# Performance work log

Hardware: AMD Instinct MI355X
Metric: run time of the kernel (lower is better)

The kernel has to match this reference:

```python
import jax, jax.numpy as jnp
import numpy as np

N = 4096      # nodes
D = 256       # input_dim
OUT = 256     # output_dim
K = 4         # num_kernels
TOPK = 16
CHEB_T = 2
ROW_TEMP = 1.0
EPS = 1e-9


def setup_inputs() -> dict:
    key = jax.random.key(0)
    ks = jax.random.split(key, 6)
    X = jax.random.normal(ks[0], (N, D), dtype=jnp.float32)
    L_k = jax.random.normal(ks[1], (K, D, D), dtype=jnp.float32) * 0.02
    alpha = jnp.ones((K,), dtype=jnp.float32)
    theta = jax.random.normal(ks[2], (CHEB_T + 1, D), dtype=jnp.float32) * 0.02
    rho_raw = jnp.zeros((), dtype=jnp.float32)
    proj_w = jax.random.normal(ks[3], (OUT, D), dtype=jnp.float32) / np.float32(np.sqrt(D))
    proj_b = jnp.zeros((OUT,), dtype=jnp.float32)
    v0 = jax.random.normal(ks[4], (N, 1), dtype=jnp.float32)  # power-iteration init
    return dict(X=X, L_k=L_k, alpha=alpha, theta=theta, rho_raw=rho_raw,
                proj_w=proj_w, proj_b=proj_b, v0=v0)


def reference(X, L_k, alpha, theta, rho_raw, proj_w, proj_b, v0):
    n, d = X.shape
    k = L_k.shape[0]
    # 1) kernel stack: A_k = X L_k X^T / sqrt(D), row softmax  -> (K,N,N)
    A = jnp.einsum('nd,kde,me->knm', X, L_k, X) / jnp.sqrt(jnp.float32(d))
    H_stack = jax.nn.softmax(A / max(ROW_TEMP, 1e-6), axis=-1)
    w = jax.nn.softmax(alpha)[:, None, None]
    H_fused = (H_stack * w).sum(0)                               # (N,N)
    # 2) soft incidence via per-row top-k + renormalize, scattered into B (N, K*N)
    vals, idx = jax.lax.top_k(H_stack, TOPK)                     # (K,N,TOPK)
    vals = vals / (vals.sum(-1, keepdims=True) + EPS)
    E = k * n
    cols = jnp.arange(k)[:, None, None] * n + jnp.arange(n)[None, :, None]
    cols = jnp.broadcast_to(cols, idx.shape)
    B = jnp.zeros((n, E), X.dtype).at[idx.reshape(-1), cols.reshape(-1)].set(vals.reshape(-1))
    W = jnp.ones((E,), X.dtype)
    # 3) hypergraph Laplacian L = I - Dv^{-1/2} B W De^{-1} B^T Dv^{-1/2}
    De = B.sum(0) + EPS
    Dv = (B * W[None, :]).sum(1) + EPS
    Dv_is = 1.0 / jnp.sqrt(Dv)
    S = (B * (W / De)[None, :]) @ B.T                            # (N,N)
    S_norm = Dv_is[:, None] * S * Dv_is[None, :]
    L = jnp.eye(n, dtype=X.dtype) - S_norm
    # 4) lambda_max via power iteration on detached L (constant, as in torch)
    Ld = jax.lax.stop_gradient(L)
    v = v0 / (jnp.linalg.norm(v0) + EPS)
    for _ in range(5):
        v = Ld @ v
        v = v / (jnp.linalg.norm(v) + EPS)
    lam = jnp.maximum((v.T @ (Ld @ v)).squeeze(), jnp.float32(1e-3))
    lam = jax.lax.stop_gradient(lam)
    # Chebyshev filter
    L_tilde = (2.0 / lam) * L - jnp.eye(n, dtype=X.dtype)
    out = X * theta[0][None, :]
    T0 = X
    T1 = L_tilde @ X
    out = out + T1 * theta[1][None, :]
    for t in range(2, CHEB_T + 1):
        T2 = 2.0 * (L_tilde @ T1) - T0
        out = out + T2 * theta[t][None, :]
        T0, T1 = T1, T2
    Z_spec = jax.nn.elu(out)
    # 5) residual blend with kernel diffusion
    Z_kern = H_fused @ X
    rho = jax.nn.sigmoid(rho_raw)
    Z_mix = rho * Z_spec + (1.0 - rho) * Z_kern
    # 6) final projection
    return Z_mix @ proj_w.T + proj_b[None, :]
```

## Files before the change

### kernel.cpp

```cpp
#include <hip/hip_runtime.h>
#include <math.h>

#define N_ 4096
#define D_ 256
#define K_ 4
#define TK_ 16
#define E_ (K_ * N_)
#define NENT_ (E_ * TK_)

typedef unsigned short u16;
typedef unsigned int u32;
typedef __attribute__((ext_vector_type(8))) short bf16x8;
typedef __attribute__((ext_vector_type(4))) float f32x4;

__device__ __forceinline__ u16 bf16_rne(float x) {
  u32 u = __float_as_uint(x);
  u32 r = u + 0x7FFFu + ((u >> 16) & 1u);
  return (u16)(r >> 16);
}


__global__ void scalars_kernel(const float* __restrict__ alpha,
                               const float* __restrict__ rho_raw,
                               float* __restrict__ scal) {
  if (threadIdx.x == 0) {
    float m = alpha[0];
    for (int k = 1; k < K_; ++k) m = fmaxf(m, alpha[k]);
    float e[K_]; float s = 0.f;
    for (int k = 0; k < K_; ++k) { e[k] = expf(alpha[k] - m); s += e[k]; }
    for (int k = 0; k < K_; ++k) scal[k] = e[k] / s;
    scal[4] = 1.0f / (1.0f + expf(-rho_raw[0]));
  }
}

__global__ void dvis_kernel(const float* __restrict__ DvAcc, float* __restrict__ Dvis) {
  int i = blockIdx.x * 256 + threadIdx.x;
  Dvis[i] = 1.0f / sqrtf(DvAcc[i] + 1e-9f);
}

__global__ void ew_scale(const float* __restrict__ M, const float* __restrict__ Dvis,
                         float* __restrict__ U) {
  int i = blockIdx.x * 256 + threadIdx.x;
  U[i] = Dvis[i >> 8] * M[i];
}

__global__ void cvt_split4(const float* __restrict__ in, u16* __restrict__ hi,
                           u16* __restrict__ lo) {
  int i = (blockIdx.x * 256 + threadIdx.x) * 4;
  float4 v = *(const float4*)(in + i);
  u16 h0 = bf16_rne(v.x), h1 = bf16_rne(v.y), h2 = bf16_rne(v.z), h3 = bf16_rne(v.w);
  float f0 = __uint_as_float((u32)h0 << 16), f1 = __uint_as_float((u32)h1 << 16);
  float f2 = __uint_as_float((u32)h2 << 16), f3 = __uint_as_float((u32)h3 << 16);
  u16 l0 = bf16_rne(v.x - f0), l1 = bf16_rne(v.y - f1);
  u16 l2 = bf16_rne(v.z - f2), l3 = bf16_rne(v.w - f3);
  *(uint2*)(hi + i) = make_uint2((u32)h0 | ((u32)h1 << 16), (u32)h2 | ((u32)h3 << 16));
  *(uint2*)(lo + i) = make_uint2((u32)l0 | ((u32)l1 << 16), (u32)l2 | ((u32)l3 << 16));
}

__global__ __launch_bounds__(256) void transpose_split(const float* __restrict__ X,
                                                       u16* __restrict__ ht,
                                                       u16* __restrict__ lt) {
  __shared__ float tile[32][33];
  const int tx = threadIdx.x & 31, ty = threadIdx.x >> 5;
  const int d0 = blockIdx.x * 32, n0 = blockIdx.y * 32;
#pragma unroll
  for (int q = 0; q < 4; ++q)
    tile[ty + q * 8][tx] = X[(size_t)(n0 + ty + q * 8) * D_ + d0 + tx];
  __syncthreads();
#pragma unroll
  for (int q = 0; q < 4; ++q) {
    int dd = ty + q * 8;
    float v = tile[tx][dd];
    u16 h = bf16_rne(v);
    float hf = __uint_as_float((u32)h << 16);
    u16 l = bf16_rne(v - hf);
    ht[(size_t)(d0 + dd) * N_ + n0 + tx] = h;
    lt[(size_t)(d0 + dd) * N_ + n0 + tx] = l;
  }
}

__global__ __launch_bounds__(256) void gemm_nn64_split(const float* __restrict__ A,
                                                       const float* __restrict__ B,
                                                       u16* __restrict__ Ch,
                                                       u16* __restrict__ Cl,
                                                       int Kdim, int lda, int ldb, int ldc) {
  __shared__ float As[16][68];
  __shared__ float Bs[16][68];
  const int tid = threadIdx.x;
  const int bm = blockIdx.x * 64, bn = blockIdx.y * 64;
  const int lrA = tid >> 2, lcA = (tid & 3) * 4;
  const int rrB = tid >> 4, ccB = (tid & 15) * 4;
  const int tx = tid & 15, ty = tid >> 4;
  const float* Ap = A + (size_t)(bm + lrA) * lda + lcA;
  const float* Bp = B + (size_t)rrB * ldb + bn + ccB;
  float acc[4][4] = {};
  for (int k0 = 0; k0 < Kdim; k0 += 16) {
    float4 av = *(const float4*)(Ap + k0);
    float4 bv = *(const float4*)(Bp + (size_t)k0 * ldb);
    __syncthreads();
    As[lcA + 0][lrA] = av.x; As[lcA + 1][lrA] = av.y;
    As[lcA + 2][lrA] = av.z; As[lcA + 3][lrA] = av.w;
    *(float4*)&Bs[rrB][ccB] = bv;
    __syncthreads();
#pragma unroll
    for (int kk = 0; kk < 16; ++kk) {
      float a[4], b[4];
      *(float4*)a = *(const float4*)&As[kk][ty * 4];
      *(float4*)b = *(const float4*)&Bs[kk][tx * 4];
#pragma unroll
      for (int i = 0; i < 4; ++i)
#pragma unroll
        for (int j = 0; j < 4; ++j) acc[i][j] += a[i] * b[j];
    }
  }
#pragma unroll
  for (int i = 0; i < 4; ++i) {
    int row = bm + ty * 4 + i;
    u16 h[4], lo[4];
#pragma unroll
    for (int j = 0; j < 4; ++j) {
      h[j] = bf16_rne(acc[i][j]);
      lo[j] = bf16_rne(acc[i][j] - __uint_as_float((u32)h[j] << 16));
    }
    size_t base = (size_t)row * ldc + bn + tx * 4;
    *(uint2*)(Ch + base) = make_uint2((u32)h[0] | ((u32)h[1] << 16), (u32)h[2] | ((u32)h[3] << 16));
    *(uint2*)(Cl + base) = make_uint2((u32)lo[0] | ((u32)lo[1] << 16), (u32)lo[2] | ((u32)lo[3] << 16));
  }
}

__global__ __launch_bounds__(256) void gemm_nt64_bias(const float* __restrict__ A,
                                                      const float* __restrict__ B,
                                                      const float* __restrict__ bias,
                                                      float* __restrict__ C,
                                                      int Kdim, int lda, int ldb, int ldc) {
  __shared__ float As[16][68];
  __shared__ float Bs[16][68];
  const int tid = threadIdx.x;
  const int bm = blockIdx.x * 64, bn = blockIdx.y * 64;
  const int lr = tid >> 2, lc = (tid & 3) * 4;
  const int tx = tid & 15, ty = tid >> 4;
  const float* Ap = A + (size_t)(bm + lr) * lda + lc;
  const float* Bp = B + (size_t)(bn + lr) * ldb + lc;
  float acc[4][4] = {};
  for (int k0 = 0; k0 < Kdim; k0 += 16) {
    float4 av = *(const float4*)(Ap + k0);
    float4 bv = *(const float4*)(Bp + k0);
    __syncthreads();
    As[lc + 0][lr] = av.x; As[lc + 1][lr] = av.y; As[lc + 2][lr] = av.z; As[lc + 3][lr] = av.w;
    Bs[lc + 0][lr] = bv.x; Bs[lc + 1][lr] = bv.y; Bs[lc + 2][lr] = bv.z; Bs[lc + 3][lr] = bv.w;
    __syncthreads();
#pragma unroll
    for (int kk = 0; kk < 16; ++kk) {
      float a[4], b[4];
      *(float4*)a = *(const float4*)&As[kk][ty * 4];
      *(float4*)b = *(const float4*)&Bs[kk][tx * 4];
#pragma unroll
      for (int i = 0; i < 4; ++i)
#pragma unroll
        for (int j = 0; j < 4; ++j) acc[i][j] += a[i] * b[j];
    }
  }
#pragma unroll
  for (int i = 0; i < 4; ++i) {
    int row = bm + ty * 4 + i;
    float4 o;
    o.x = acc[i][0] + bias[bn + tx * 4 + 0];
    o.y = acc[i][1] + bias[bn + tx * 4 + 1];
    o.z = acc[i][2] + bias[bn + tx * 4 + 2];
    o.w = acc[i][3] + bias[bn + tx * 4 + 3];
    *(float4*)(C + (size_t)row * ldc + bn + tx * 4) = o;
  }
}


__global__ __launch_bounds__(256) void scores_mfma(const u16* __restrict__ Ahg,
                                                   const u16* __restrict__ Alg,
                                                   const u16* __restrict__ Bhg,
                                                   const u16* __restrict__ Blg,
                                                   float* __restrict__ C, float scale) {
  __shared__ char smem[32768];
  char* pAh = smem;
  char* pAl = smem + 16384;
  const int tid = threadIdx.x;
  const int bm = blockIdx.x * 128, bn = blockIdx.y * 128;
  const int w = tid >> 6, l = tid & 63;
  const int wr = (w >> 1) * 64, wc = (w & 1) * 64;
  const int srow = tid >> 3, scol = (tid & 7) * 8;
  const int lb = l & 15, lke = (l >> 4) * 8;
  const u16* bh0 = Bhg + (size_t)(bn + wc + 0  + lb) * D_ + lke;
  const u16* bh1 = Bhg + (size_t)(bn + wc + 16 + lb) * D_ + lke;
  const u16* bh2 = Bhg + (size_t)(bn + wc + 32 + lb) * D_ + lke;
  const u16* bh3 = Bhg + (size_t)(bn + wc + 48 + lb) * D_ + lke;
  const size_t dlo = (size_t)(Blg - Bhg);
  f32x4 acc[4][4];
#pragma unroll
  for (int i = 0; i < 4; ++i)
#pragma unroll
    for (int j = 0; j < 4; ++j) { acc[i][j][0] = 0.f; acc[i][j][1] = 0.f; acc[i][j][2] = 0.f; acc[i][j][3] = 0.f; }

  for (int c = 0; c < 4; ++c) {
    const int k0 = c * 64;
    uint4 ah[4], al[4];
#pragma unroll
    for (int ii = 0; ii < 4; ++ii) {
      int r = srow + ii * 32;
      ah[ii] = *(const uint4*)(Ahg + (size_t)(bm + r) * D_ + k0 + scol);
      al[ii] = *(const uint4*)(Alg + (size_t)(bm + r) * D_ + k0 + scol);
    }
    __syncthreads();
#pragma unroll
    for (int ii = 0; ii < 4; ++ii) {
      int r = srow + ii * 32;
      int off = r * 128 + ((scol * 2) ^ ((r & 7) << 4));
      *(uint4*)(pAh + off) = ah[ii];
      *(uint4*)(pAl + off) = al[ii];
    }
    __syncthreads();
#pragma unroll
    for (int kk = 0; kk < 2; ++kk) {
      const int kb = kk * 64 + ((l >> 4) << 4);
      const int ge = k0 + kk * 32;
      bf16x8 fbh[4], fbl[4];
      fbh[0] = *(const bf16x8*)(bh0 + ge); fbl[0] = *(const bf16x8*)(bh0 + dlo + ge);
      fbh[1] = *(const bf16x8*)(bh1 + ge); fbl[1] = *(const bf16x8*)(bh1 + dlo + ge);
      fbh[2] = *(const bf16x8*)(bh2 + ge); fbl[2] = *(const bf16x8*)(bh2 + dlo + ge);
      fbh[3] = *(const bf16x8*)(bh3 + ge); fbl[3] = *(const bf16x8*)(bh3 + dlo + ge);
#pragma unroll
      for (int i = 0; i < 4; ++i) {
        int ra = wr + i * 16 + lb;
        int oa = ra * 128 + (kb ^ ((ra & 7) << 4));
        bf16x8 fah = *(const bf16x8*)(pAh + oa);
        bf16x8 fal = *(const bf16x8*)(pAl + oa);
#pragma unroll
        for (int j = 0; j < 4; ++j) {
          acc[i][j] = __builtin_amdgcn_mfma_f32_16x16x32_bf16(fah, fbh[j], acc[i][j], 0, 0, 0);
          acc[i][j] = __builtin_amdgcn_mfma_f32_16x16x32_bf16(fah, fbl[j], acc[i][j], 0, 0, 0);
          acc[i][j] = __builtin_amdgcn_mfma_f32_16x16x32_bf16(fal, fbh[j], acc[i][j], 0, 0, 0);
        }
      }
    }
  }
  float* Cs = (float*)smem;
  const int cr = (l >> 4) * 4, cc = l & 15;
#pragma unroll
  for (int p = 0; p < 2; ++p) {
    __syncthreads();
    if ((w >> 1) == p) {
#pragma unroll
      for (int i = 0; i < 4; ++i)
#pragma unroll
        for (int r = 0; r < 4; ++r) {
          int rl = i * 16 + cr + r;
          int sw = ((rl >> 2) & 3) << 4;
#pragma unroll
          for (int j = 0; j < 4; ++j) {
            int cl = wc + j * 16 + cc;
            Cs[rl * 128 + (cl ^ sw)] = acc[i][j][r] * scale;
          }
        }
    }
    __syncthreads();
#pragma unroll
    for (int ii = 0; ii < 8; ++ii) {
      int rl = ii * 8 + (tid >> 5);
      int c4 = (tid & 31) * 4;
      float4 v = *(float4*)&Cs[rl * 128 + (c4 ^ (((rl >> 2) & 3) << 4))];
      *(float4*)(C + (size_t)(bm + p * 64 + rl) * N_ + bn + c4) = v;
    }
  }
}

__global__ __launch_bounds__(256) void zkern_mfma(const float* __restrict__ S,
                                                  const float* __restrict__ rowmax,
                                                  const float* __restrict__ rowZ,
                                                  const u16* __restrict__ BhT,
                                                  const u16* __restrict__ BlT,
                                                  float* __restrict__ Zpart,
                                                  const float* __restrict__ scal,
                                                  int kidx, int kchunk) {
  __shared__ char smem[32768];
  char* pAh = smem;
  char* pAl = smem + 16384;
  const int tid = threadIdx.x;
  const int bm = blockIdx.x * 128, bn = blockIdx.y * 128;
  const int kz = blockIdx.z;
  const int w = tid >> 6, l = tid & 63;
  const int wr = (w >> 1) * 64, wc = (w & 1) * 64;
  const int arow = tid >> 4, acol = (tid & 15) * 4;
  const int lb = l & 15, lke = (l >> 4) * 8;
  const u16* bh0 = BhT + (size_t)(bn + wc + 0  + lb) * N_ + lke;
  const u16* bh1 = BhT + (size_t)(bn + wc + 16 + lb) * N_ + lke;
  const u16* bh2 = BhT + (size_t)(bn + wc + 32 + lb) * N_ + lke;
  const u16* bh3 = BhT + (size_t)(bn + wc + 48 + lb) * N_ + lke;
  const size_t dlo = (size_t)(BlT - BhT);
  float rm[8];
#pragma unroll
  for (int ii = 0; ii < 8; ++ii) rm[ii] = rowmax[bm + arow + ii * 16];
  f32x4 acc[4][4];
#pragma unroll
  for (int i = 0; i < 4; ++i)
#pragma unroll
    for (int j = 0; j < 4; ++j) { acc[i][j][0] = 0.f; acc[i][j][1] = 0.f; acc[i][j][2] = 0.f; acc[i][j][3] = 0.f; }

  const int nchunk = kchunk >> 6;
  for (int c = 0; c < nchunk; ++c) {
    const int k0 = kz * kchunk + c * 64;
    uint2 eh[8], el[8];
#pragma unroll
    for (int ii = 0; ii < 8; ++ii) {
      int r = arow + ii * 16;
      float4 s = *(const float4*)(S + (size_t)(bm + r) * N_ + k0 + acol);
      float e0 = expf(s.x - rm[ii]), e1 = expf(s.y - rm[ii]);
      float e2 = expf(s.z - rm[ii]), e3 = expf(s.w - rm[ii]);
      u16 h0 = bf16_rne(e0), h1 = bf16_rne(e1), h2 = bf16_rne(e2), h3 = bf16_rne(e3);
      u16 l0 = bf16_rne(e0 - __uint_as_float((u32)h0 << 16));
      u16 l1 = bf16_rne(e1 - __uint_as_float((u32)h1 << 16));
      u16 l2 = bf16_rne(e2 - __uint_as_float((u32)h2 << 16));
      u16 l3 = bf16_rne(e3 - __uint_as_float((u32)h3 << 16));
      eh[ii] = make_uint2((u32)h0 | ((u32)h1 << 16), (u32)h2 | ((u32)h3 << 16));
      el[ii] = make_uint2((u32)l0 | ((u32)l1 << 16), (u32)l2 | ((u32)l3 << 16));
    }
    __syncthreads();
#pragma unroll
    for (int ii = 0; ii < 8; ++ii) {
      int r = arow + ii * 16;
      int off = r * 128 + ((acol * 2) ^ ((r & 7) << 4));
      *(uint2*)(pAh + off) = eh[ii];
      *(uint2*)(pAl + off) = el[ii];
    }
    __syncthreads();
#pragma unroll
    for (int kk = 0; kk < 2; ++kk) {
      const int kb = kk * 64 + ((l >> 4) << 4);
      const int ge = k0 + kk * 32;
      bf16x8 fbh[4], fbl[4];
      fbh[0] = *(const bf16x8*)(bh0 + ge); fbl[0] = *(const bf16x8*)(bh0 + dlo + ge);
      fbh[1] = *(const bf16x8*)(bh1 + ge); fbl[1] = *(const bf16x8*)(bh1 + dlo + ge);
      fbh[2] = *(const bf16x8*)(bh2 + ge); fbl[2] = *(const bf16x8*)(bh2 + dlo + ge);
      fbh[3] = *(const bf16x8*)(bh3 + ge); fbl[3] = *(const bf16x8*)(bh3 + dlo + ge);
#pragma unroll
      for (int i = 0; i < 4; ++i) {
        int ra = wr + i * 16 + lb;
        int oa = ra * 128 + (kb ^ ((ra & 7) << 4));
        bf16x8 fah = *(const bf16x8*)(pAh + oa);
        bf16x8 fal = *(const bf16x8*)(pAl + oa);
#pragma unroll
        for (int j = 0; j < 4; ++j) {
          acc[i][j] = __builtin_amdgcn_mfma_f32_16x16x32_bf16(fah, fbh[j], acc[i][j], 0, 0, 0);
          acc[i][j] = __builtin_amdgcn_mfma_f32_16x16x32_bf16(fah, fbl[j], acc[i][j], 0, 0, 0);
          acc[i][j] = __builtin_amdgcn_mfma_f32_16x16x32_bf16(fal, fbh[j], acc[i][j], 0, 0, 0);
        }
      }
    }
  }
  const float wk = scal[kidx];
  float* Zp = Zpart + (size_t)kz * N_ * D_;
  float* Cs = (float*)smem;
  const int cr = (l >> 4) * 4, cc = l & 15;
#pragma unroll
  for (int p = 0; p < 2; ++p) {
    __syncthreads();
    if ((w >> 1) == p) {
#pragma unroll
      for (int i = 0; i < 4; ++i)
#pragma unroll
        for (int r = 0; r < 4; ++r) {
          int rl = i * 16 + cr + r;
          int sw = ((rl >> 2) & 3) << 4;
#pragma unroll
          for (int j = 0; j < 4; ++j) {
            int cl = wc + j * 16 + cc;
            Cs[rl * 128 + (cl ^ sw)] = acc[i][j][r];
          }
        }
    }
    __syncthreads();
#pragma unroll
    for (int ii = 0; ii < 8; ++ii) {
      int rl = ii * 8 + (tid >> 5);
      int c4 = (tid & 31) * 4;
      int row = bm + p * 64 + rl;
      float sc = wk / rowZ[row];
      float4 v = *(float4*)&Cs[rl * 128 + (c4 ^ (((rl >> 2) & 3) << 4))];
      float* zb = Zp + (size_t)row * D_ + bn + c4;
      float4 z = *(float4*)zb;
      z.x += sc * v.x; z.y += sc * v.y; z.z += sc * v.z; z.w += sc * v.w;
      *(float4*)zb = z;
    }
  }
}

__global__ __launch_bounds__(256) void rowstats_topk(const float* __restrict__ S,
                                                     float* __restrict__ rowmax,
                                                     float* __restrict__ rowZ,
                                                     float* __restrict__ tkv,
                                                     int* __restrict__ tki) {
  const int row = blockIdx.x, tid = threadIdx.x;
  const int wid = tid >> 6, lane = tid & 63;
  __shared__ int hist[1024];
  __shared__ int P[256];
  __shared__ float cval[256];
  __shared__ int cgi[256];
  __shared__ int ccnt;
  __shared__ int binlo_s;
  __shared__ float rv[4];
  __shared__ float stk[TK_];
  __shared__ int itk[TK_];
  __shared__ float tv16[TK_];
  __shared__ float mzs[3];

  hist[tid] = 0; hist[tid + 256] = 0; hist[tid + 512] = 0; hist[tid + 768] = 0;
  if (tid == 0) ccnt = 0;

  const float4* Sp = (const float4*)(S + (size_t)row * N_);
  float r[16];
  float lmax = -3.4e38f;
#pragma unroll
  for (int it = 0; it < 4; ++it) {
    float4 v = Sp[tid + it * 256];
    r[it * 4 + 0] = v.x; r[it * 4 + 1] = v.y; r[it * 4 + 2] = v.z; r[it * 4 + 3] = v.w;
    lmax = fmaxf(lmax, fmaxf(fmaxf(v.x, v.y), fmaxf(v.z, v.w)));
  }
#pragma unroll
  for (int off = 32; off; off >>= 1) lmax = fmaxf(lmax, __shfl_xor(lmax, off));
  if (lane == 0) rv[wid] = lmax;
  __syncthreads();
  if (tid == 0) mzs[0] = fmaxf(fmaxf(rv[0], rv[1]), fmaxf(rv[2], rv[3]));
  __syncthreads();
  const float M = mzs[0];
  float ls = 0.f;
#pragma unroll
  for (int j = 0; j < 16; ++j) ls += expf(r[j] - M);
#pragma unroll
  for (int off = 32; off; off >>= 1) ls += __shfl_xor(ls, off);
  if (lane == 0) rv[wid] = ls;
  __syncthreads();
  if (tid == 0) {
    float z = rv[0] + rv[1] + rv[2] + rv[3];
    mzs[1] = z; rowmax[row] = M; rowZ[row] = z;
  }
  __syncthreads();
  const float Z = mzs[1];

#pragma unroll
  for (int j = 0; j < 16; ++j) {
    u32 u = __float_as_uint(r[j]);
    u32 key = (u >> 31) ? ~u : (u | 0x80000000u);
    atomicAdd(&hist[key >> 22], 1);
  }
  __syncthreads();
  const int b0 = tid * 4;
  const int h0 = hist[b0], h1 = hist[b0 + 1], h2 = hist[b0 + 2], h3 = hist[b0 + 3];
  P[tid] = h0 + h1 + h2 + h3;
  __syncthreads();
  for (int o = 1; o < 256; o <<= 1) {
    int v = P[tid] + ((tid + o < 256) ? P[tid + o] : 0);
    __syncthreads();
    P[tid] = v;
    __syncthreads();
  }
  {
    int above = (tid < 255) ? P[tid + 1] : 0;
    int s3 = above + h3, s2 = s3 + h2, s1 = s2 + h1, s0 = s1 + h0;
    if (s3 >= TK_ && above < TK_) binlo_s = b0 + 3;
    else if (s2 >= TK_ && s3 < TK_) binlo_s = b0 + 2;
    else if (s1 >= TK_ && s2 < TK_) binlo_s = b0 + 1;
    else if (s0 >= TK_ && s1 < TK_) binlo_s = b0;
  }
  __syncthreads();
  const u32 kmin = (u32)binlo_s << 22;
#pragma unroll
  for (int j = 0; j < 16; ++j) {
    u32 u = __float_as_uint(r[j]);
    u32 key = (u >> 31) ? ~u : (u | 0x80000000u);
    if (key >= kmin) {
      int p = atomicAdd(&ccnt, 1);
      if (p < 256) {
        cval[p] = r[j];
        cgi[p] = 4 * tid + ((j >> 2) << 10) + (j & 3);
      }
    }
  }
  __syncthreads();
  const int nc = min(ccnt, 256);
  for (int t = 0; t < TK_; ++t) {
    if (tid < 64) {
      float bv = -3.4e38f; int bg = 0x7fffffff, bp = -1;
      for (int p = tid; p < nc; p += 64) {
        float v = cval[p]; int g = cgi[p];
        if (v > bv || (v == bv && g < bg)) { bv = v; bg = g; bp = p; }
      }
#pragma unroll
      for (int off = 32; off; off >>= 1) {
        float ov = __shfl_xor(bv, off);
        int og = __shfl_xor(bg, off);
        int op = __shfl_xor(bp, off);
        if (ov > bv || (ov == bv && og < bg)) { bv = ov; bg = og; bp = op; }
      }
      if (tid == 0) { stk[t] = bv; itk[t] = bg; cval[bp] = -3.4e38f; }
    }
    __syncthreads();
  }
  if (tid < TK_) tv16[tid] = expf(stk[tid] - M) / Z;
  __syncthreads();
  if (tid == 0) { float s = 0.f; for (int q = 0; q < TK_; ++q) s += tv16[q]; mzs[2] = s + 1e-9f; }
  __syncthreads();
  if (tid < TK_) {
    tkv[(size_t)row * TK_ + tid] = tv16[tid] / mzs[2];
    tki[(size_t)row * TK_ + tid] = itk[tid];
  }
}

__global__ void edge_scan(const float* __restrict__ tkv, const int* __restrict__ tki,
                          float* __restrict__ DvAcc, int* __restrict__ cnt,
                          float* __restrict__ invDe) {
  int e = blockIdx.x * 256 + threadIdx.x;
  float s = 0.f;
#pragma unroll
  for (int q = 0; q < TK_; ++q) s += tkv[(size_t)e * TK_ + q];
  invDe[e] = 1.0f / (s + 1e-9f);
#pragma unroll
  for (int q = 0; q < TK_; ++q) {
    int m = tki[(size_t)e * TK_ + q];
    atomicAdd(&DvAcc[m], tkv[(size_t)e * TK_ + q]);
    atomicAdd(&cnt[m], 1);
  }
}

__global__ __launch_bounds__(1024) void scan_offsets(const int* __restrict__ cnt,
                                                     int* __restrict__ off,
                                                     int* __restrict__ cur) {
  __shared__ int part[1024];
  const int t = threadIdx.x;
  const int b = t * 4;
  int c0 = cnt[b], c1 = cnt[b + 1], c2 = cnt[b + 2], c3 = cnt[b + 3];
  part[t] = c0 + c1 + c2 + c3;
  __syncthreads();
  for (int o = 1; o < 1024; o <<= 1) {
    int v = part[t] + ((t >= o) ? part[t - o] : 0);
    __syncthreads();
    part[t] = v;
    __syncthreads();
  }
  int ex = (t == 0) ? 0 : part[t - 1];
  off[b] = ex; off[b + 1] = ex + c0; off[b + 2] = ex + c0 + c1; off[b + 3] = ex + c0 + c1 + c2;
  cur[b] = off[b]; cur[b + 1] = off[b + 1]; cur[b + 2] = off[b + 2]; cur[b + 3] = off[b + 3];
  if (t == 1023) off[N_] = part[1023];
}

__global__ void edge_fill(const float* __restrict__ tkv, const int* __restrict__ tki,
                          int* __restrict__ cur, int* __restrict__ ince,
                          float* __restrict__ incv) {
  int e = blockIdx.x * 256 + threadIdx.x;
#pragma unroll
  for (int q = 0; q < TK_; ++q) {
    int m = tki[(size_t)e * TK_ + q];
    int pos = atomicAdd(&cur[m], 1);
    ince[pos] = e;
    incv[pos] = tkv[(size_t)e * TK_ + q];
  }
}

__global__ void pi_init(const float* __restrict__ v0, const float* __restrict__ Dvis,
                        float* __restrict__ v, float* __restrict__ u) {
  int i = blockIdx.x * 256 + threadIdx.x;
  float x = v0[i];
  v[i] = x; u[i] = Dvis[i] * x;
}

__global__ void pi_ye(const float* __restrict__ u, const float* __restrict__ tkv,
                      const int* __restrict__ tki, const float* __restrict__ invDe,
                      float* __restrict__ ye) {
  int e = blockIdx.x * 256 + threadIdx.x;
  const float* tv = tkv + (size_t)e * TK_;
  const int* ti = tki + (size_t)e * TK_;
  float a = 0.f;
#pragma unroll
  for (int q = 0; q < TK_; ++q) a += tv[q] * u[ti[q]];
  ye[e] = a * invDe[e];
}

__global__ void pi_step(const float* __restrict__ v, const float* __restrict__ ye,
                        const int* __restrict__ off, const int* __restrict__ ince,
                        const float* __restrict__ incv, const float* __restrict__ Dvis,
                        float* __restrict__ vn, float* __restrict__ un) {
  int m = blockIdx.x * 256 + threadIdx.x;
  float z = 0.f;
  int j0 = off[m], j1 = off[m + 1];
  for (int j = j0; j < j1; ++j) z += incv[j] * ye[ince[j]];
  float wv = v[m] - Dvis[m] * z;
  vn[m] = wv; un[m] = Dvis[m] * wv;
}

__global__ __launch_bounds__(256) void pi_final(const float* __restrict__ v,
                                                const float* __restrict__ ye,
                                                const int* __restrict__ off,
                                                const int* __restrict__ ince,
                                                const float* __restrict__ incv,
                                                const float* __restrict__ Dvis,
                                                float* __restrict__ partial) {
  __shared__ float r1[256], r2[256];
  int m = blockIdx.x * 256 + threadIdx.x;
  float z = 0.f;
  int j0 = off[m], j1 = off[m + 1];
  for (int j = j0; j < j1; ++j) z += incv[j] * ye[ince[j]];
  float wv = v[m] - Dvis[m] * z;
  r1[threadIdx.x] = v[m] * wv;
  r2[threadIdx.x] = v[m] * v[m];
  __syncthreads();
  for (int s = 128; s; s >>= 1) {
    if (threadIdx.x < s) { r1[threadIdx.x] += r1[threadIdx.x + s]; r2[threadIdx.x] += r2[threadIdx.x + s]; }
    __syncthreads();
  }
  if (threadIdx.x == 0) { partial[blockIdx.x * 2] = r1[0]; partial[blockIdx.x * 2 + 1] = r2[0]; }
}

__global__ void pi_lam(const float* __restrict__ partial, float* __restrict__ scal) {
  if (threadIdx.x == 0) {
    float s1 = 0.f, s2 = 0.f;
    for (int b = 0; b < N_ / 256; ++b) { s1 += partial[2 * b]; s2 += partial[2 * b + 1]; }
    scal[5] = fmaxf(s1 / s2, 1e-3f);
  }
}

__global__ __launch_bounds__(256) void ye_mat(const float* __restrict__ U,
                                              const float* __restrict__ tkv,
                                              const int* __restrict__ tki,
                                              const float* __restrict__ invDe,
                                              float* __restrict__ Ye) {
  const int e = blockIdx.x, d = threadIdx.x;
  __shared__ float sv[TK_];
  __shared__ int si[TK_];
  if (d < TK_) { sv[d] = tkv[(size_t)e * TK_ + d]; si[d] = tki[(size_t)e * TK_ + d]; }
  __syncthreads();
  float a = 0.f;
#pragma unroll
  for (int q = 0; q < TK_; ++q) a += sv[q] * U[(size_t)si[q] * D_ + d];
  Ye[(size_t)e * D_ + d] = a * invDe[e];
}

__global__ __launch_bounds__(256) void bgather_combine(const float* __restrict__ Ye,
                                                       const int* __restrict__ off,
                                                       const int* __restrict__ ince,
                                                       const float* __restrict__ incv,
                                                       const float* __restrict__ Dvis,
                                                       const float* __restrict__ Mx,
                                                       const float* __restrict__ G,
                                                       const float* __restrict__ scal,
                                                       float* __restrict__ out, int mode) {
  const int m = blockIdx.x, d = threadIdx.x;
  const int j0 = off[m], j1 = off[m + 1];
  float z = 0.f;
  for (int j = j0; j < j1; ++j) z += incv[j] * Ye[(size_t)ince[j] * D_ + d];
  const float lam = scal[5];
  const float c = 2.0f / lam;
  const size_t idx = (size_t)m * D_ + d;
  const float zz = Dvis[m] * z;
  float r;
  if (mode == 1) r = (c - 1.0f) * Mx[idx] - c * zz;
  else           r = (2.0f * c - 2.0f) * Mx[idx] - 2.0f * c * zz - G[idx];
  out[idx] = r;
}

__global__ void mix_kernel(const float* __restrict__ X, const float* __restrict__ T1,
                           const float* __restrict__ T2, const float* __restrict__ theta,
                           const float* __restrict__ Zpart, int splitk,
                           const float* __restrict__ scal, float* __restrict__ Zmix) {
  const int i = blockIdx.x * 256 + threadIdx.x;
  const int d = i & (D_ - 1);
  float cheb = X[i] * theta[d] + T1[i] * theta[D_ + d] + T2[i] * theta[2 * D_ + d];
  float zs = cheb > 0.f ? cheb : expm1f(cheb);
  float zk = 0.f;
  for (int s = 0; s < splitk; ++s) zk += Zpart[(size_t)s * N_ * D_ + i];
  const float rho = scal[4];
  Zmix[i] = rho * zs + (1.0f - rho) * zk;
}


extern "C" void kernel_launch(void* const* d_in, const int* in_sizes, int n_in,
                              void* d_out, int out_size, void* d_ws, size_t ws_size,
                              hipStream_t stream) {
  const float* X       = (const float*)d_in[0];
  const float* L_k     = (const float*)d_in[1];
  const float* alpha   = (const float*)d_in[2];
  const float* theta   = (const float*)d_in[3];
  const float* rho_raw = (const float*)d_in[4];
  const float* proj_w  = (const float*)d_in[5];
  const float* proj_b  = (const float*)d_in[6];
  const float* v0      = (const float*)d_in[7];
  float* out = (float*)d_out;

  char* w = (char*)d_ws;
  size_t o = 0;
  auto alloc = [&](size_t bytes) -> char* {
    char* p = w + o; o += (bytes + 255) & ~(size_t)255; return p;
  };
  float* S     = (float*)alloc((size_t)N_ * N_ * 4);
  u16*   Xh    = (u16*)  alloc((size_t)N_ * D_ * 2);
  u16*   Xl    = (u16*)  alloc((size_t)N_ * D_ * 2);
  u16*   XhT   = (u16*)  alloc((size_t)D_ * N_ * 2);
  u16*   XlT   = (u16*)  alloc((size_t)D_ * N_ * 2);
  u16*   XLh   = (u16*)  alloc((size_t)N_ * D_ * 2);
  u16*   XLl   = (u16*)  alloc((size_t)N_ * D_ * 2);
  float* rowmax= (float*)alloc(N_ * 4);
  float* rowZ  = (float*)alloc(N_ * 4);
  float* tkv   = (float*)alloc((size_t)NENT_ * 4);
  int*   tki   = (int*)  alloc((size_t)NENT_ * 4);
  float* invDe = (float*)alloc(E_ * 4);
  float* DvAcc = (float*)alloc(N_ * 4);
  float* Dvis  = (float*)alloc(N_ * 4);
  int*   cnt   = (int*)  alloc(N_ * 4);
  int*   off   = (int*)  alloc((N_ + 1) * 4);
  int*   cur   = (int*)  alloc(N_ * 4);
  int*   ince  = (int*)  alloc((size_t)NENT_ * 4);
  float* incv  = (float*)alloc((size_t)NENT_ * 4);
  float* va    = (float*)alloc(N_ * 4);
  float* ua    = (float*)alloc(N_ * 4);
  float* vbuf  = (float*)alloc(N_ * 4);
  float* ubuf  = (float*)alloc(N_ * 4);
  float* yev   = (float*)alloc(E_ * 4);
  float* part  = (float*)alloc((N_ / 256) * 2 * 4);
  float* scal  = (float*)alloc(256);
  int SPLITK = 8;
  while (SPLITK > 1 && o + (size_t)SPLITK * N_ * D_ * 4 > ws_size) SPLITK >>= 1;
  float* Zpart = (float*)alloc((size_t)SPLITK * N_ * D_ * 4);
  const int kchunk = N_ / SPLITK;
  float* U    = S;
  float* Ye   = S + (size_t)N_ * D_;
  float* T1   = Ye + (size_t)E_ * D_;
  float* T2   = T1 + (size_t)N_ * D_;
  float* Zmix = T2 + (size_t)N_ * D_;

  scalars_kernel<<<1, 64, 0, stream>>>(alpha, rho_raw, scal);
  hipMemsetAsync(Zpart, 0, (size_t)SPLITK * N_ * D_ * 4, stream);
  hipMemsetAsync(DvAcc, 0, N_ * 4, stream);
  hipMemsetAsync(cnt, 0, N_ * 4, stream);

  cvt_split4<<<(N_ * D_ / 4) / 256, 256, 0, stream>>>(X, Xh, Xl);
  transpose_split<<<dim3(D_ / 32, N_ / 32), 256, 0, stream>>>(X, XhT, XlT);

  for (int k = 0; k < K_; ++k) {
    gemm_nn64_split<<<dim3(N_ / 64, D_ / 64), 256, 0, stream>>>(
        X, L_k + (size_t)k * D_ * D_, XLh, XLl, D_, D_, D_, D_);
    scores_mfma<<<dim3(N_ / 128, N_ / 128), 256, 0, stream>>>(
        XLh, XLl, Xh, Xl, S, 1.0f / 16.0f);
    rowstats_topk<<<N_, 256, 0, stream>>>(
        S, rowmax, rowZ, tkv + (size_t)k * N_ * TK_, tki + (size_t)k * N_ * TK_);
    zkern_mfma<<<dim3(N_ / 128, D_ / 128, SPLITK), 256, 0, stream>>>(
        S, rowmax, rowZ, XhT, XlT, Zpart, scal, k, kchunk);
  }

  edge_scan<<<E_ / 256, 256, 0, stream>>>(tkv, tki, DvAcc, cnt, invDe);
  dvis_kernel<<<N_ / 256, 256, 0, stream>>>(DvAcc, Dvis);
  scan_offsets<<<1, 1024, 0, stream>>>(cnt, off, cur);
  edge_fill<<<E_ / 256, 256, 0, stream>>>(tkv, tki, cur, ince, incv);

  pi_init<<<N_ / 256, 256, 0, stream>>>(v0, Dvis, va, ua);
  float* vc = va; float* uc = ua; float* vn = vbuf; float* un = ubuf;
  for (int it = 0; it < 5; ++it) {
    pi_ye<<<E_ / 256, 256, 0, stream>>>(uc, tkv, tki, invDe, yev);
    pi_step<<<N_ / 256, 256, 0, stream>>>(vc, yev, off, ince, incv, Dvis, vn, un);
    float* tv = vc; vc = vn; vn = tv;
    float* tu = uc; uc = un; un = tu;
  }
  pi_ye<<<E_ / 256, 256, 0, stream>>>(uc, tkv, tki, invDe, yev);
  pi_final<<<N_ / 256, 256, 0, stream>>>(vc, yev, off, ince, incv, Dvis, part);
  pi_lam<<<1, 64, 0, stream>>>(part, scal);

  ew_scale<<<N_ * D_ / 256, 256, 0, stream>>>(X, Dvis, U);
  ye_mat<<<E_, 256, 0, stream>>>(U, tkv, tki, invDe, Ye);
  bgather_combine<<<N_, 256, 0, stream>>>(Ye, off, ince, incv, Dvis, X, X, scal, T1, 1);
  ew_scale<<<N_ * D_ / 256, 256, 0, stream>>>(T1, Dvis, U);
  ye_mat<<<E_, 256, 0, stream>>>(U, tkv, tki, invDe, Ye);
  bgather_combine<<<N_, 256, 0, stream>>>(Ye, off, ince, incv, Dvis, T1, X, scal, T2, 2);

  mix_kernel<<<N_ * D_ / 256, 256, 0, stream>>>(X, T1, T2, theta, Zpart, SPLITK, scal, Zmix);

  gemm_nt64_bias<<<dim3(N_ / 64, D_ / 64), 256, 0, stream>>>(
      Zmix, proj_w, proj_b, out, D_, D_, D_, D_);
}
```

Before: 1.449 ms.

## Double-buffer LDS A-tiles in scores and zkern MFMA kernels

Both MFMA GEMM kernels now keep two LDS buffers for the A operand. The next chunk's global loads (and, in zkern, its exp/bf16 split) are issued before the current chunk's MFMAs and stored into the alternate buffer afterwards. This cuts one barrier per iteration and is meant to hide global-load latency behind matrix math. In exchange, LDS per block doubles to 64KB and register pressure rises, which may lower occupancy.

Result: faster. 1.276 ms (-11.9%).

```diff
diff --git a/kernel.cpp b/kernel.cpp
--- a/kernel.cpp
+++ b/kernel.cpp
@@ -178,9 +178,7 @@
                                                    const u16* __restrict__ Bhg,
                                                    const u16* __restrict__ Blg,
                                                    float* __restrict__ C, float scale) {
-  __shared__ char smem[32768];
-  char* pAh = smem;
-  char* pAl = smem + 16384;
+  __shared__ char smem[65536];
   const int tid = threadIdx.x;
   const int bm = blockIdx.x * 128, bn = blockIdx.y * 128;
   const int w = tid >> 6, l = tid & 63;
@@ -192,34 +190,51 @@
   const u16* bh2 = Bhg + (size_t)(bn + wc + 32 + lb) * D_ + lke;
   const u16* bh3 = Bhg + (size_t)(bn + wc + 48 + lb) * D_ + lke;
   const size_t dlo = (size_t)(Blg - Bhg);
+  const int aoff[4] = {
+    (srow + 0)  * 128 + ((scol * 2) ^ (((srow + 0)  & 7) << 4)),
+    (srow + 32) * 128 + ((scol * 2) ^ (((srow + 32) & 7) << 4)),
+    (srow + 64) * 128 + ((scol * 2) ^ (((srow + 64) & 7) << 4)),
+    (srow + 96) * 128 + ((scol * 2) ^ (((srow + 96) & 7) << 4)) };
   f32x4 acc[4][4];
 #pragma unroll
   for (int i = 0; i < 4; ++i)
 #pragma unroll
     for (int j = 0; j < 4; ++j) { acc[i][j][0] = 0.f; acc[i][j][1] = 0.f; acc[i][j][2] = 0.f; acc[i][j][3] = 0.f; }
 
+  uint4 ah[4], al[4];
+#pragma unroll
+  for (int ii = 0; ii < 4; ++ii) {
+    int r = srow + ii * 32;
+    ah[ii] = *(const uint4*)(Ahg + (size_t)(bm + r) * D_ + scol);
+    al[ii] = *(const uint4*)(Alg + (size_t)(bm + r) * D_ + scol);
+  }
+  {
+    char* bAh = smem; char* bAl = smem + 16384;
+#pragma unroll
+    for (int ii = 0; ii < 4; ++ii) {
+      *(uint4*)(bAh + aoff[ii]) = ah[ii];
+      *(uint4*)(bAl + aoff[ii]) = al[ii];
+    }
+  }
+  __syncthreads();
+
   for (int c = 0; c < 4; ++c) {
-    const int k0 = c * 64;
-    uint4 ah[4], al[4];
-#pragma unroll
-    for (int ii = 0; ii < 4; ++ii) {
-      int r = srow + ii * 32;
-      ah[ii] = *(const uint4*)(Ahg + (size_t)(bm + r) * D_ + k0 + scol);
-      al[ii] = *(const uint4*)(Alg + (size_t)(bm + r) * D_ + k0 + scol);
-    }
-    __syncthreads();
-#pragma unroll
-    for (int ii = 0; ii < 4; ++ii) {
-      int r = srow + ii * 32;
-      int off = r * 128 + ((scol * 2) ^ ((r & 7) << 4));
-      *(uint4*)(pAh + off) = ah[ii];
-      *(uint4*)(pAl + off) = al[ii];
-    }
-    __syncthreads();
+    char* bAh = smem + ((c & 1) << 15);
+    char* bAl = bAh + 16384;
+    const bool hn = (c < 3);
+    if (hn) {
+      const int kn = (c + 1) * 64;
+#pragma unroll
+      for (int ii = 0; ii < 4; ++ii) {
+        int r = srow + ii * 32;
+        ah[ii] = *(const uint4*)(Ahg + (size_t)(bm + r) * D_ + kn + scol);
+        al[ii] = *(const uint4*)(Alg + (size_t)(bm + r) * D_ + kn + scol);
+      }
+    }
 #pragma unroll
     for (int kk = 0; kk < 2; ++kk) {
       const int kb = kk * 64 + ((l >> 4) << 4);
-      const int ge = k0 + kk * 32;
+      const int ge = c * 64 + kk * 32;
       bf16x8 fbh[4], fbl[4];
       fbh[0] = *(const bf16x8*)(bh0 + ge); fbl[0] = *(const bf16x8*)(bh0 + dlo + ge);
       fbh[1] = *(const bf16x8*)(bh1 + ge); fbl[1] = *(const bf16x8*)(bh1 + dlo + ge);
@@ -229,8 +244,8 @@
       for (int i = 0; i < 4; ++i) {
         int ra = wr + i * 16 + lb;
         int oa = ra * 128 + (kb ^ ((ra & 7) << 4));
-        bf16x8 fah = *(const bf16x8*)(pAh + oa);
-        bf16x8 fal = *(const bf16x8*)(pAl + oa);
+        bf16x8 fah = *(const bf16x8*)(bAh + oa);
+        bf16x8 fal = *(const bf16x8*)(bAl + oa);
 #pragma unroll
         for (int j = 0; j < 4; ++j) {
           acc[i][j] = __builtin_amdgcn_mfma_f32_16x16x32_bf16(fah, fbh[j], acc[i][j], 0, 0, 0);
@@ -239,6 +254,16 @@
         }
       }
     }
+    if (hn) {
+      char* nAh = smem + (((c + 1) & 1) << 15);
+      char* nAl = nAh + 16384;
+#pragma unroll
+      for (int ii = 0; ii < 4; ++ii) {
+        *(uint4*)(nAh + aoff[ii]) = ah[ii];
+        *(uint4*)(nAl + aoff[ii]) = al[ii];
+      }
+    }
+    __syncthreads();
   }
   float* Cs = (float*)smem;
   const int cr = (l >> 4) * 4, cc = l & 15;
@@ -278,9 +303,7 @@
                                                   float* __restrict__ Zpart,
                                                   const float* __restrict__ scal,
                                                   int kidx, int kchunk) {
-  __shared__ char smem[32768];
-  char* pAh = smem;
-  char* pAl = smem + 16384;
+  __shared__ char smem[65536];
   const int tid = threadIdx.x;
   const int bm = blockIdx.x * 128, bn = blockIdx.y * 128;
   const int kz = blockIdx.z;
@@ -294,8 +317,13 @@
   const u16* bh3 = BhT + (size_t)(bn + wc + 48 + lb) * N_ + lke;
   const size_t dlo = (size_t)(BlT - BhT);
   float rm[8];
-#pragma unroll
-  for (int ii = 0; ii < 8; ++ii) rm[ii] = rowmax[bm + arow + ii * 16];
+  int aoff[8];
+#pragma unroll
+  for (int ii = 0; ii < 8; ++ii) {
+    int r = arow + ii * 16;
+    rm[ii] = rowmax[bm + r];
+    aoff[ii] = r * 128 + ((acol * 2) ^ ((r & 7) << 4));
+  }
   f32x4 acc[4][4];
 #pragma unroll
   for (int i = 0; i < 4; ++i)
@@ -303,36 +331,43 @@
     for (int j = 0; j < 4; ++j) { acc[i][j][0] = 0.f; acc[i][j][1] = 0.f; acc[i][j][2] = 0.f; acc[i][j][3] = 0.f; }
 
   const int nchunk = kchunk >> 6;
-  for (int c = 0; c < nchunk; ++c) {
-    const int k0 = kz * kchunk + c * 64;
-    uint2 eh[8], el[8];
+  const int kbase = kz * kchunk;
+
+  float4 sv[8];
+#pragma unroll
+  for (int ii = 0; ii < 8; ++ii)
+    sv[ii] = *(const float4*)(S + (size_t)(bm + arow + ii * 16) * N_ + kbase + acol);
+  {
+    char* bAh = smem; char* bAl = smem + 16384;
 #pragma unroll
     for (int ii = 0; ii < 8; ++ii) {
-      int r = arow + ii * 16;
-      float4 s = *(const float4*)(S + (size_t)(bm + r) * N_ + k0 + acol);
-      float e0 = expf(s.x - rm[ii]), e1 = expf(s.y - rm[ii]);
-      float e2 = expf(s.z - rm[ii]), e3 = expf(s.w - rm[ii]);
+      float e0 = expf(sv[ii].x - rm[ii]), e1 = expf(sv[ii].y - rm[ii]);
+      float e2 = expf(sv[ii].z - rm[ii]), e3 = expf(sv[ii].w - rm[ii]);
       u16 h0 = bf16_rne(e0), h1 = bf16_rne(e1), h2 = bf16_rne(e2), h3 = bf16_rne(e3);
       u16 l0 = bf16_rne(e0 - __uint_as_float((u32)h0 << 16));
       u16 l1 = bf16_rne(e1 - __uint_as_float((u32)h1 << 16));
       u16 l2 = bf16_rne(e2 - __uint_as_float((u32)h2 << 16));
       u16 l3 = bf16_rne(e3 - __uint_as_float((u32)h3 << 16));
-      eh[ii] = make_uint2((u32)h0 | ((u32)h1 << 16), (u32)h2 | ((u32)h3 << 16));
-      el[ii] = make_uint2((u32)l0 | ((u32)l1 << 16), (u32)l2 | ((u32)l3 << 16));
-    }
-    __syncthreads();
-#pragma unroll
-    for (int ii = 0; ii < 8; ++ii) {
-      int r = arow + ii * 16;
-      int off = r * 128 + ((acol * 2) ^ ((r & 7) << 4));
-      *(uint2*)(pAh + off) = eh[ii];
-      *(uint2*)(pAl + off) = el[ii];
-    }
-    __syncthreads();
+      *(uint2*)(bAh + aoff[ii]) = make_uint2((u32)h0 | ((u32)h1 << 16), (u32)h2 | ((u32)h3 << 16));
+      *(uint2*)(bAl + aoff[ii]) = make_uint2((u32)l0 | ((u32)l1 << 16), (u32)l2 | ((u32)l3 << 16));
+    }
+  }
+  __syncthreads();
+
+  for (int c = 0; c < nchunk; ++c) {
+    char* bAh = smem + ((c & 1) << 15);
+    char* bAl = bAh + 16384;
+    const bool hn = (c + 1 < nchunk);
+    if (hn) {
+      const int kn = kbase + (c + 1) * 64;
+#pragma unroll
+      for (int ii = 0; ii < 8; ++ii)
+        sv[ii] = *(const float4*)(S + (size_t)(bm + arow + ii * 16) * N_ + kn + acol);
+    }
 #pragma unroll
     for (int kk = 0; kk < 2; ++kk) {
       const int kb = kk * 64 + ((l >> 4) << 4);
-      const int ge = k0 + kk * 32;
+      const int ge = kbase + c * 64 + kk * 32;
       bf16x8 fbh[4], fbl[4];
       fbh[0] = *(const bf16x8*)(bh0 + ge); fbl[0] = *(const bf16x8*)(bh0 + dlo + ge);
       fbh[1] = *(const bf16x8*)(bh1 + ge); fbl[1] = *(const bf16x8*)(bh1 + dlo + ge);
@@ -342,8 +377,8 @@
       for (int i = 0; i < 4; ++i) {
         int ra = wr + i * 16 + lb;
         int oa = ra * 128 + (kb ^ ((ra & 7) << 4));
-        bf16x8 fah = *(const bf16x8*)(pAh + oa);
-        bf16x8 fal = *(const bf16x8*)(pAl + oa);
+        bf16x8 fah = *(const bf16x8*)(bAh + oa);
+        bf16x8 fal = *(const bf16x8*)(bAl + oa);
 #pragma unroll
         for (int j = 0; j < 4; ++j) {
           acc[i][j] = __builtin_amdgcn_mfma_f32_16x16x32_bf16(fah, fbh[j], acc[i][j], 0, 0, 0);
@@ -352,6 +387,23 @@
         }
       }
     }
+    if (hn) {
+      char* nAh = smem + (((c + 1) & 1) << 15);
+      char* nAl = nAh + 16384;
+#pragma unroll
+      for (int ii = 0; ii < 8; ++ii) {
+        float e0 = expf(sv[ii].x - rm[ii]), e1 = expf(sv[ii].y - rm[ii]);
+        float e2 = expf(sv[ii].z - rm[ii]), e3 = expf(sv[ii].w - rm[ii]);
+        u16 h0 = bf16_rne(e0), h1 = bf16_rne(e1), h2 = bf16_rne(e2), h3 = bf16_rne(e3);
+        u16 l0 = bf16_rne(e0 - __uint_as_float((u32)h0 << 16));
+        u16 l1 = bf16_rne(e1 - __uint_as_float((u32)h1 << 16));
+        u16 l2 = bf16_rne(e2 - __uint_as_float((u32)h2 << 16));
+        u16 l3 = bf16_rne(e3 - __uint_as_float((u32)h3 << 16));
+        *(uint2*)(nAh + aoff[ii]) = make_uint2((u32)h0 | ((u32)h1 << 16), (u32)h2 | ((u32)h3 << 16));
+        *(uint2*)(nAl + aoff[ii]) = make_uint2((u32)l0 | ((u32)l1 << 16), (u32)l2 | ((u32)l3 << 16));
+      }
+    }
+    __syncthreads();
   }
   const float wk = scal[kidx];
   float* Zp = Zpart + (size_t)kz * N_ * D_;
```
